# Kernel tuning notes

Hardware: AMD Instinct MI355X
Metric: run time of the kernel (lower is better)

Reference implementation:

```python
import jax, jax.numpy as jnp
import numpy as np


def _binarize(x):
    # sign binarization to {-1, +1}; sign(0) -> +1
    return jnp.where(x >= 0, 1.0, -1.0).astype(x.dtype)


def setup_inputs() -> dict:
    key = jax.random.key(0)
    kx, kw, kb = jax.random.split(key, 3)
    C_in, C_out, K = 128, 128, 3
    x = jax.random.normal(kx, (32, C_in, 112, 112), dtype=jnp.float32)
    # conv weight [C_out, C_in, K, K], kaiming-ish scale
    W = jax.random.normal(kw, (C_out, C_in, K, K), dtype=jnp.float32) * (1.0 / np.sqrt(C_in * K * K))
    b = jax.random.normal(kb, (C_out,), dtype=jnp.float32) * 0.01
    return {"x": x, "W": W, "b": b}


def reference(x, W, b):
    # BinConv: binarize activations, binarize weights, then standard conv2d
    xb = _binarize(x)                # [N, C_in, H, W] in {-1, +1}
    Wb = _binarize(W)                # [C_out, C_in, K, K] in {-1, +1}
    out = jax.lax.conv_general_dilated(
        xb, Wb,
        window_strides=(1, 1),
        padding=((1, 1), (1, 1)),
        rhs_dilation=(1, 1),
        dimension_numbers=("NCHW", "OIHW", "NCHW"),
    )
    return out + b[None, :, None, None]
```

## Files before the change

### kernel.cpp

```cpp
#include <hip/hip_runtime.h>
#include <stdint.h>

#define Hdim 112
#define Wdim 112
#define CIN  128
#define COUT 128
#define NB   32
#define HW   (Hdim*Wdim)
#define HALO_W 114
#define ROWSTR (HALO_W*16)
#define SLOT_STRIDE (4*ROWSTR)
#define IT 2


typedef int   v4i __attribute__((ext_vector_type(4)));
typedef int  v16i __attribute__((ext_vector_type(16)));
typedef float v4f __attribute__((ext_vector_type(4)));

__global__ void pack_w_i8(const float* __restrict__ W, char* __restrict__ Wi8) {
    int t = blockIdx.x * blockDim.x + threadIdx.x;
    if (t >= COUT * 9) return;
    int co = t / 9, tap = t % 9;
    const float* wp = W + (size_t)co * CIN * 9 + tap;
    uint32_t* dst = (uint32_t*)(Wi8 + ((size_t)tap * COUT + co) * CIN);
    #pragma unroll
    for (int c4 = 0; c4 < 32; c4++) {
        uint32_t word = 0;
        #pragma unroll
        for (int j = 0; j < 4; j++) {
            uint32_t neg = __float_as_uint(wp[(size_t)(c4 * 4 + j) * 9]) >> 31;
            word |= (neg ? 0xFFu : 0x01u) << (8 * j);
        }
        dst[c4] = word;
    }
}

__global__ __launch_bounds__(256) void pack_x_kernel(const float* __restrict__ x,
                                                     uint4* __restrict__ pkx) {
    int gid = blockIdx.x * blockDim.x + threadIdx.x;
    int n = gid / (HW / 4);
    int p = (gid - n * (HW / 4)) * 4;
    const float* xp = x + (size_t)n * CIN * HW + p;
    uint32_t m[4][4] = {{0,0,0,0},{0,0,0,0},{0,0,0,0},{0,0,0,0}};
    #pragma unroll
    for (int c = 0; c < CIN; c++) {
        v4f v = __builtin_nontemporal_load(
            reinterpret_cast<const v4f*>(xp + (size_t)c * HW));
        int q = c >> 5, s = c & 31;
        m[0][q] |= (__float_as_uint(v.x) >> 31) << s;
        m[1][q] |= (__float_as_uint(v.y) >> 31) << s;
        m[2][q] |= (__float_as_uint(v.z) >> 31) << s;
        m[3][q] |= (__float_as_uint(v.w) >> 31) << s;
    }
    uint4* op = pkx + (size_t)n * HW + p;
    #pragma unroll
    for (int j = 0; j < 4; j++)
        op[j] = make_uint4(m[j][0], m[j][1], m[j][2], m[j][3]);
}

__device__ __forceinline__ uint32_t expand4(uint32_t b) {
    uint32_t s = ((b & 0xFu) * 0x00204081u) & 0x01010101u;
    return 0x01010101u ^ (s * 0xFEu);
}

__device__ __forceinline__ void stage_px(const uint4* __restrict__ pkx, char* halo,
                                         int n, int h, int w, int ring, int c) {
    bool valid = (h >= 0) && (h < Hdim) && (w >= 0) && (w < Wdim);
    uint32_t keep = valid ? 0xFFFFFFFFu : 0u;
    int hc = min(max(h, 0), Hdim - 1);
    int wc = min(max(w, 0), Wdim - 1);
    uint4 bits = pkx[(size_t)n * HW + hc * Wdim + wc];
    uint32_t src[4] = {bits.x, bits.y, bits.z, bits.w};
    unsigned base = (unsigned)(ring * ROWSTR + c * 16);
    #pragma unroll
    for (int sl = 0; sl < 8; sl++) {
        uint32_t q = src[sl >> 1] >> ((sl & 1) * 16);
        uint4 ov;
        ov.x = expand4(q)       & keep;
        ov.y = expand4(q >> 4)  & keep;
        ov.z = expand4(q >> 8)  & keep;
        ov.w = expand4(q >> 12) & keep;
        *reinterpret_cast<uint4*>(&halo[sl * SLOT_STRIDE + base]) = ov;
    }
}

__global__ __launch_bounds__(256, 2) void binconv_mfma(
    const uint4* __restrict__ pkx, const char* __restrict__ Wi8,
    const float* __restrict__ bias, float* __restrict__ out) {
    __shared__ char halo[8 * SLOT_STRIDE];

    int tid = threadIdx.x;
    int hy = blockIdx.x;
    int n  = blockIdx.y;
    int h0 = hy * (2 * IT);

    for (int i = tid; i < 4 * HALO_W; i += 256) {
        int r = i / HALO_W, c = i - r * HALO_W;
        stage_px(pkx, halo, n, h0 - 1 + r, c - 1, r, c);
    }

    int wid = tid >> 6, l = tid & 63;
    int al = l & 31, ah = l >> 5;
    int cobase = wid * 32;

    int colb[7], rsel[7], wcol[7];
    #pragma unroll
    for (int pt = 0; pt < 7; pt++) {
        int P = pt * 32 + al;
        rsel[pt] = (P >= Wdim) ? 1 : 0;
        wcol[pt] = P - rsel[pt] * Wdim;
        colb[pt] = wcol[pt] * 16 + ah * SLOT_STRIDE;
    }

    const char* wA = Wi8 + ((size_t)cobase + al) * CIN + ah * 16;
    float* ob = out + (size_t)n * COUT * HW;

    __syncthreads();

    #pragma unroll
    for (int s = 0; s < IT; s++) {
        const int hs = h0 + 2 * s;

        v16i acc[7];
        #pragma unroll
        for (int pt = 0; pt < 7; pt++)
            #pragma unroll
            for (int i = 0; i < 16; i++) acc[pt][i] = 0;

        v4i A[4];
        #pragma unroll
        for (int kk = 0; kk < 4; kk++)
            A[kk] = *reinterpret_cast<const v4i*>(wA + kk * 32);

        #pragma unroll
        for (int tap = 0; tap < 9; tap++) {
            v4i N[4];
            if (tap < 8) {
                const char* wt = wA + (size_t)(tap + 1) * COUT * CIN;
                #pragma unroll
                for (int kk = 0; kk < 4; kk++)
                    N[kk] = *reinterpret_cast<const v4i*>(wt + kk * 32);
            }
            const int dy = tap / 3, dx = tap % 3;
            int po[7];
            #pragma unroll
            for (int pt = 0; pt < 7; pt++)
                po[pt] = colb[pt] + (((2 * s + dy + rsel[pt]) & 3) * ROWSTR) + dx * 16;
            #pragma unroll
            for (int kk = 0; kk < 4; kk++) {
                v4i b[7];
                #pragma unroll
                for (int pt = 0; pt < 7; pt++)
                    b[pt] = *reinterpret_cast<const v4i*>(&halo[kk * 2 * SLOT_STRIDE + po[pt]]);
                #pragma unroll
                for (int pt = 0; pt < 7; pt++)
                    acc[pt] = __builtin_amdgcn_mfma_i32_32x32x32_i8(A[kk], b[pt], acc[pt], 0, 0, 0);
            }
            if (tap < 8) {
                #pragma unroll
                for (int kk = 0; kk < 4; kk++) A[kk] = N[kk];
            }
        }

        #pragma unroll
        for (int reg = 0; reg < 16; reg++) {
            int co = cobase + (reg & 3) + ((reg >> 2) << 3) + (ah << 2);
            float bv = bias[co];
            #pragma unroll
            for (int pt = 0; pt < 7; pt++) {
                size_t off = (size_t)co * HW + (size_t)(hs + rsel[pt]) * Wdim + wcol[pt];
                __builtin_nontemporal_store((float)acc[pt][reg] + bv, &ob[off]);
            }
        }

        if (s + 1 < IT) {
            asm volatile("s_waitcnt lgkmcnt(0)" ::: "memory");
            __builtin_amdgcn_s_barrier();
            __builtin_amdgcn_sched_barrier(0);
            for (int i = tid; i < 2 * HALO_W; i += 256) {
                int r = i / HALO_W, c = i - r * HALO_W;
                stage_px(pkx, halo, n, hs + 3 + r, c - 1, (2 * s + r) & 3, c);
            }
            asm volatile("s_waitcnt lgkmcnt(0)" ::: "memory");
            __builtin_amdgcn_s_barrier();
            __builtin_amdgcn_sched_barrier(0);
        }
    }
}

extern "C" void kernel_launch(void* const* d_in, const int* in_sizes, int n_in,
                              void* d_out, int out_size, void* d_ws, size_t ws_size,
                              hipStream_t stream) {
    const float* x = (const float*)d_in[0];
    const float* W = (const float*)d_in[1];
    const float* b = (const float*)d_in[2];
    float* out = (float*)d_out;
    char* ws = (char*)d_ws;
    char*  Wi8 = ws;
    uint4* pkx = (uint4*)(ws + 147456);

    pack_w_i8<<<dim3((COUT * 9 + 255) / 256), dim3(256), 0, stream>>>(W, Wi8);
    pack_x_kernel<<<dim3(NB * HW / 4 / 256), dim3(256), 0, stream>>>(x, pkx);
    binconv_mfma<<<dim3(Hdim / (2 * IT), NB), dim3(256), 0, stream>>>(pkx, Wi8, b, out);
}
```

Before: 124.2 us.

## Switch binary conv MFMA to 16x16x64 i8 tiles with 2D wave split

Result: slower. 165.6 us (+33.3%).

```diff
diff --git a/kernel.cpp b/kernel.cpp
--- a/kernel.cpp
+++ b/kernel.cpp
@@ -14,7 +14,6 @@
 
 
 typedef int   v4i __attribute__((ext_vector_type(4)));
-typedef int  v16i __attribute__((ext_vector_type(16)));
 typedef float v4f __attribute__((ext_vector_type(4)));
 
 __global__ void pack_w_i8(const float* __restrict__ W, char* __restrict__ Wi8) {
@@ -100,19 +99,11 @@
     }
 
     int wid = tid >> 6, l = tid & 63;
-    int al = l & 31, ah = l >> 5;
-    int cobase = wid * 32;
+    int l16 = l & 15, lk = l >> 4;
+    int cobase = (wid & 1) * 64;
+    int wrow   = wid >> 1;
 
-    int colb[7], rsel[7], wcol[7];
-    #pragma unroll
-    for (int pt = 0; pt < 7; pt++) {
-        int P = pt * 32 + al;
-        rsel[pt] = (P >= Wdim) ? 1 : 0;
-        wcol[pt] = P - rsel[pt] * Wdim;
-        colb[pt] = wcol[pt] * 16 + ah * SLOT_STRIDE;
-    }
-
-    const char* wA = Wi8 + ((size_t)cobase + al) * CIN + ah * 16;
+    const char* wA = Wi8 + ((size_t)(cobase + l16)) * CIN + lk * 16;
     float* ob = out + (size_t)n * COUT * HW;
 
     __syncthreads();
@@ -121,55 +112,53 @@
     for (int s = 0; s < IT; s++) {
         const int hs = h0 + 2 * s;
 
-        v16i acc[7];
+        v4i acc[4][7];
         #pragma unroll
-        for (int pt = 0; pt < 7; pt++)
+        for (int ct = 0; ct < 4; ct++)
             #pragma unroll
-            for (int i = 0; i < 16; i++) acc[pt][i] = 0;
-
-        v4i A[4];
-        #pragma unroll
-        for (int kk = 0; kk < 4; kk++)
-            A[kk] = *reinterpret_cast<const v4i*>(wA + kk * 32);
+            for (int pt = 0; pt < 7; pt++)
+                #pragma unroll
+                for (int i = 0; i < 4; i++) acc[ct][pt][i] = 0;
 
         #pragma unroll
         for (int tap = 0; tap < 9; tap++) {
-            v4i N[4];
-            if (tap < 8) {
-                const char* wt = wA + (size_t)(tap + 1) * COUT * CIN;
+            const int dy = tap / 3, dx = tap % 3;
+            const unsigned rbase =
+                (unsigned)(((2 * s + wrow + dy) & 3) * ROWSTR + dx * 16 + l16 * 16);
+            const char* wt = wA + (size_t)tap * COUT * CIN;
+            v4i A[4][2];
+            #pragma unroll
+            for (int ct = 0; ct < 4; ct++)
                 #pragma unroll
-                for (int kk = 0; kk < 4; kk++)
-                    N[kk] = *reinterpret_cast<const v4i*>(wt + kk * 32);
-            }
-            const int dy = tap / 3, dx = tap % 3;
-            int po[7];
+                for (int kk = 0; kk < 2; kk++)
+                    A[ct][kk] = *reinterpret_cast<const v4i*>(
+                        wt + (size_t)ct * 16 * CIN + kk * 64);
             #pragma unroll
-            for (int pt = 0; pt < 7; pt++)
-                po[pt] = colb[pt] + (((2 * s + dy + rsel[pt]) & 3) * ROWSTR) + dx * 16;
-            #pragma unroll
-            for (int kk = 0; kk < 4; kk++) {
-                v4i b[7];
+            for (int kk = 0; kk < 2; kk++) {
+                const unsigned sb = (unsigned)((kk * 4 + lk) * SLOT_STRIDE) + rbase;
                 #pragma unroll
-                for (int pt = 0; pt < 7; pt++)
-                    b[pt] = *reinterpret_cast<const v4i*>(&halo[kk * 2 * SLOT_STRIDE + po[pt]]);
-                #pragma unroll
-                for (int pt = 0; pt < 7; pt++)
-                    acc[pt] = __builtin_amdgcn_mfma_i32_32x32x32_i8(A[kk], b[pt], acc[pt], 0, 0, 0);
-            }
-            if (tap < 8) {
-                #pragma unroll
-                for (int kk = 0; kk < 4; kk++) A[kk] = N[kk];
+                for (int pt = 0; pt < 7; pt++) {
+                    v4i b = *reinterpret_cast<const v4i*>(&halo[sb + pt * 256]);
+                    acc[0][pt] = __builtin_amdgcn_mfma_i32_16x16x64_i8(A[0][kk], b, acc[0][pt], 0, 0, 0);
+                    acc[1][pt] = __builtin_amdgcn_mfma_i32_16x16x64_i8(A[1][kk], b, acc[1][pt], 0, 0, 0);
+                    acc[2][pt] = __builtin_amdgcn_mfma_i32_16x16x64_i8(A[2][kk], b, acc[2][pt], 0, 0, 0);
+                    acc[3][pt] = __builtin_amdgcn_mfma_i32_16x16x64_i8(A[3][kk], b, acc[3][pt], 0, 0, 0);
+                }
             }
         }
 
+        const int hrow = hs + wrow;
         #pragma unroll
-        for (int reg = 0; reg < 16; reg++) {
-            int co = cobase + (reg & 3) + ((reg >> 2) << 3) + (ah << 2);
-            float bv = bias[co];
+        for (int ct = 0; ct < 4; ct++) {
             #pragma unroll
-            for (int pt = 0; pt < 7; pt++) {
-                size_t off = (size_t)co * HW + (size_t)(hs + rsel[pt]) * Wdim + wcol[pt];
-                __builtin_nontemporal_store((float)acc[pt][reg] + bv, &ob[off]);
+            for (int reg = 0; reg < 4; reg++) {
+                int co = cobase + ct * 16 + lk * 4 + reg;
+                float bv = bias[co];
+                #pragma unroll
+                for (int pt = 0; pt < 7; pt++) {
+                    size_t off = (size_t)co * HW + (size_t)hrow * Wdim + pt * 16 + l16;
+                    __builtin_nontemporal_store((float)acc[ct][pt][reg] + bv, &ob[off]);
+                }
             }
         }
 
```

## Fuse activation binarization into conv kernel halo staging

Applied to the files above, without the earlier changes.

After: 317.1 us. 155% more time.

```diff
diff --git a/kernel.cpp b/kernel.cpp
--- a/kernel.cpp
+++ b/kernel.cpp
@@ -14,7 +14,6 @@
 
 
 typedef int   v4i __attribute__((ext_vector_type(4)));
-typedef int  v16i __attribute__((ext_vector_type(16)));
 typedef float v4f __attribute__((ext_vector_type(4)));
 
 __global__ void pack_w_i8(const float* __restrict__ W, char* __restrict__ Wi8) {
@@ -35,46 +34,28 @@
     }
 }
 
-__global__ __launch_bounds__(256) void pack_x_kernel(const float* __restrict__ x,
-                                                     uint4* __restrict__ pkx) {
-    int gid = blockIdx.x * blockDim.x + threadIdx.x;
-    int n = gid / (HW / 4);
-    int p = (gid - n * (HW / 4)) * 4;
-    const float* xp = x + (size_t)n * CIN * HW + p;
-    uint32_t m[4][4] = {{0,0,0,0},{0,0,0,0},{0,0,0,0},{0,0,0,0}};
-    #pragma unroll
-    for (int c = 0; c < CIN; c++) {
-        v4f v = __builtin_nontemporal_load(
-            reinterpret_cast<const v4f*>(xp + (size_t)c * HW));
-        int q = c >> 5, s = c & 31;
-        m[0][q] |= (__float_as_uint(v.x) >> 31) << s;
-        m[1][q] |= (__float_as_uint(v.y) >> 31) << s;
-        m[2][q] |= (__float_as_uint(v.z) >> 31) << s;
-        m[3][q] |= (__float_as_uint(v.w) >> 31) << s;
-    }
-    uint4* op = pkx + (size_t)n * HW + p;
-    #pragma unroll
-    for (int j = 0; j < 4; j++)
-        op[j] = make_uint4(m[j][0], m[j][1], m[j][2], m[j][3]);
-}
-
 __device__ __forceinline__ uint32_t expand4(uint32_t b) {
     uint32_t s = ((b & 0xFu) * 0x00204081u) & 0x01010101u;
     return 0x01010101u ^ (s * 0xFEu);
 }
 
-__device__ __forceinline__ void stage_px(const uint4* __restrict__ pkx, char* halo,
-                                         int n, int h, int w, int ring, int c) {
+__device__ __forceinline__ void stage_px_f32(const float* __restrict__ xn,
+                                             char* halo, int h, int w,
+                                             int ring, int c) {
     bool valid = (h >= 0) && (h < Hdim) && (w >= 0) && (w < Wdim);
     uint32_t keep = valid ? 0xFFFFFFFFu : 0u;
     int hc = min(max(h, 0), Hdim - 1);
     int wc = min(max(w, 0), Wdim - 1);
-    uint4 bits = pkx[(size_t)n * HW + hc * Wdim + wc];
-    uint32_t src[4] = {bits.x, bits.y, bits.z, bits.w};
+    const float* p = xn + hc * Wdim + wc;
     unsigned base = (unsigned)(ring * ROWSTR + c * 16);
     #pragma unroll
     for (int sl = 0; sl < 8; sl++) {
-        uint32_t q = src[sl >> 1] >> ((sl & 1) * 16);
+        uint32_t q = 0;
+        #pragma unroll
+        for (int j = 0; j < 16; j++) {
+            float v = __builtin_nontemporal_load(p + (size_t)(sl * 16 + j) * HW);
+            q |= (__float_as_uint(v) >> 31) << j;
+        }
         uint4 ov;
         ov.x = expand4(q)       & keep;
         ov.y = expand4(q >> 4)  & keep;
@@ -85,7 +66,7 @@
 }
 
 __global__ __launch_bounds__(256, 2) void binconv_mfma(
-    const uint4* __restrict__ pkx, const char* __restrict__ Wi8,
+    const float* __restrict__ x, const char* __restrict__ Wi8,
     const float* __restrict__ bias, float* __restrict__ out) {
     __shared__ char halo[8 * SLOT_STRIDE];
 
@@ -94,9 +75,11 @@
     int n  = blockIdx.y;
     int h0 = hy * (2 * IT);
 
+    const float* xn = x + (size_t)n * CIN * HW;
+
     for (int i = tid; i < 4 * HALO_W; i += 256) {
         int r = i / HALO_W, c = i - r * HALO_W;
-        stage_px(pkx, halo, n, h0 - 1 + r, c - 1, r, c);
+        stage_px_f32(xn, halo, h0 - 1 + r, c - 1, r, c);
     }
 
     int wid = tid >> 6, l = tid & 63;
@@ -121,6 +104,8 @@
     for (int s = 0; s < IT; s++) {
         const int hs = h0 + 2 * s;
 
+        v16i_decl:;
+        typedef int v16i __attribute__((ext_vector_type(16)));
         v16i acc[7];
         #pragma unroll
         for (int pt = 0; pt < 7; pt++)
@@ -179,7 +164,7 @@
             __builtin_amdgcn_sched_barrier(0);
             for (int i = tid; i < 2 * HALO_W; i += 256) {
                 int r = i / HALO_W, c = i - r * HALO_W;
-                stage_px(pkx, halo, n, hs + 3 + r, c - 1, (2 * s + r) & 3, c);
+                stage_px_f32(xn, halo, hs + 3 + r, c - 1, (2 * s + r) & 3, c);
             }
             asm volatile("s_waitcnt lgkmcnt(0)" ::: "memory");
             __builtin_amdgcn_s_barrier();
@@ -195,11 +180,8 @@
     const float* W = (const float*)d_in[1];
     const float* b = (const float*)d_in[2];
     float* out = (float*)d_out;
-    char* ws = (char*)d_ws;
-    char*  Wi8 = ws;
-    uint4* pkx = (uint4*)(ws + 147456);
+    char* Wi8 = (char*)d_ws;
 
     pack_w_i8<<<dim3((COUT * 9 + 255) / 256), dim3(256), 0, stream>>>(W, Wi8);
-    pack_x_kernel<<<dim3(NB * HW / 4 / 256), dim3(256), 0, stream>>>(x, pkx);
-    binconv_mfma<<<dim3(Hdim / (2 * IT), NB), dim3(256), 0, stream>>>(pkx, Wi8, b, out);
+    binconv_mfma<<<dim3(Hdim / (2 * IT), NB), dim3(256), 0, stream>>>(x, Wi8, b, out);
 }
```

## Reuse one LDS halo read across three horizontal taps via DPP lane shifts

Applied to the files above, without the earlier changes.

Result: slower. 137.9 us (+11.0%).

```diff
diff --git a/kernel.cpp b/kernel.cpp
--- a/kernel.cpp
+++ b/kernel.cpp
@@ -102,6 +102,8 @@
     int wid = tid >> 6, l = tid & 63;
     int al = l & 31, ah = l >> 5;
     int cobase = wid * 32;
+    const bool eL = (l & 15) == 0;
+    const bool eR = (l & 15) == 15;
 
     int colb[7], rsel[7], wcol[7];
     #pragma unroll
@@ -127,38 +129,43 @@
             #pragma unroll
             for (int i = 0; i < 16; i++) acc[pt][i] = 0;
 
-        v4i A[4];
-        #pragma unroll
-        for (int kk = 0; kk < 4; kk++)
-            A[kk] = *reinterpret_cast<const v4i*>(wA + kk * 32);
-
-        #pragma unroll
-        for (int tap = 0; tap < 9; tap++) {
-            v4i N[4];
-            if (tap < 8) {
-                const char* wt = wA + (size_t)(tap + 1) * COUT * CIN;
+        #pragma unroll
+        for (int dy = 0; dy < 3; dy++) {
+            v4i A[3][4];
+            #pragma unroll
+            for (int t = 0; t < 3; t++)
                 #pragma unroll
                 for (int kk = 0; kk < 4; kk++)
-                    N[kk] = *reinterpret_cast<const v4i*>(wt + kk * 32);
-            }
-            const int dy = tap / 3, dx = tap % 3;
-            int po[7];
+                    A[t][kk] = *reinterpret_cast<const v4i*>(
+                        wA + (size_t)(3 * dy + t) * COUT * CIN + kk * 32);
+
+            int poc[7];
             #pragma unroll
             for (int pt = 0; pt < 7; pt++)
-                po[pt] = colb[pt] + (((2 * s + dy + rsel[pt]) & 3) * ROWSTR) + dx * 16;
+                poc[pt] = colb[pt] + (((2 * s + dy + rsel[pt]) & 3) * ROWSTR) + 16;
+
             #pragma unroll
             for (int kk = 0; kk < 4; kk++) {
-                v4i b[7];
+                const int sb = kk * 2 * SLOT_STRIDE;
                 #pragma unroll
-                for (int pt = 0; pt < 7; pt++)
-                    b[pt] = *reinterpret_cast<const v4i*>(&halo[kk * 2 * SLOT_STRIDE + po[pt]]);
-                #pragma unroll
-                for (int pt = 0; pt < 7; pt++)
-                    acc[pt] = __builtin_amdgcn_mfma_i32_32x32x32_i8(A[kk], b[pt], acc[pt], 0, 0, 0);
-            }
-            if (tap < 8) {
-                #pragma unroll
-                for (int kk = 0; kk < 4; kk++) A[kk] = N[kk];
+                for (int pt = 0; pt < 7; pt++) {
+                    v4i bc = *reinterpret_cast<const v4i*>(&halo[sb + poc[pt]]);
+                    v4i bp = bc;
+                    if (eL | eR)
+                        bp = *reinterpret_cast<const v4i*>(
+                            &halo[sb + poc[pt] + (eL ? -16 : 16)]);
+                    v4i bl, br;
+                    #pragma unroll
+                    for (int i = 0; i < 4; i++) {
+                        bl[i] = __builtin_amdgcn_update_dpp(
+                            bp[i], bc[i], 0x111, 0xf, 0xf, false);
+                        br[i] = __builtin_amdgcn_update_dpp(
+                            bp[i], bc[i], 0x101, 0xf, 0xf, false);
+                    }
+                    acc[pt] = __builtin_amdgcn_mfma_i32_32x32x32_i8(A[0][kk], bl, acc[pt], 0, 0, 0);
+                    acc[pt] = __builtin_amdgcn_mfma_i32_32x32x32_i8(A[1][kk], bc, acc[pt], 0, 0, 0);
+                    acc[pt] = __builtin_amdgcn_mfma_i32_32x32x32_i8(A[2][kk], br, acc[pt], 0, 0, 0);
+                }
             }
         }
 
```
